# Optimization experiments

Measured on AMD Instinct MI355X. Metric: run time of the kernel, lower is better.

## Reference

```python
import jax, jax.numpy as jnp
import numpy as np
import math

NEG_INF = -10000.0

def setup_inputs() -> dict:
    key = jax.random.key(0)
    k1, k2, k3 = jax.random.split(key, 3)
    B, Sq, Sk, H, D = 2, 2048, 2048, 16, 64
    q = jax.random.normal(k1, (B, Sq, H, D), dtype=jnp.float32)
    kv = jax.random.normal(k2, (B, Sk, 2, H, D), dtype=jnp.float32)
    key_padding_mask = jax.random.randint(k3, (B, Sk), 0, 2).astype(jnp.bool_)
    return {"q": q, "kv": kv, "key_padding_mask": key_padding_mask}

def reference(q, kv, key_padding_mask):
    # q: (B, Sq, H, D); kv: (B, Sk, 2, H, D); key_padding_mask: (B, Sk) True=keep
    D = q.shape[-1]
    softmax_scale = 1.0 / math.sqrt(D)
    k = kv[:, :, 0]  # (B, Sk, H, D)
    v = kv[:, :, 1]  # (B, Sk, H, D)
    # (B, H, Sq, Sk) score matrix
    scores = jnp.einsum('bthd,bshd->bhts', q, k * softmax_scale)
    # additive padding mask: 0 where keep, NEG_INF where masked out
    pad = jnp.where(key_padding_mask, 0.0, NEG_INF).astype(scores.dtype)
    scores = scores + pad[:, None, None, :]
    attention = jax.nn.softmax(scores, axis=-1)
    # dropout_p = 0.0 (eval mode) -> no-op
    output = jnp.einsum('bhts,bshd->bthd', attention, v)
    return output
```

## Files before the change

kernel.cpp:

```cpp
#include <hip/hip_runtime.h>

typedef unsigned short u16;
typedef unsigned int   u32;
typedef u16   u16x8 __attribute__((ext_vector_type(8)));
typedef float f32x4 __attribute__((ext_vector_type(4)));
typedef __bf16 bf16x8 __attribute__((ext_vector_type(8)));
typedef u32   u32x2 __attribute__((ext_vector_type(2)));
typedef u32   u32x4 __attribute__((ext_vector_type(4)));

#define QSCALE  0.18033688011112f
#define BM_OPEN  -28.8539008177793f
#define BM_MASK  -14455.8043097f

__device__ __forceinline__ u16 f2bf(float x){
  __bf16 h = (__bf16)x;
  return __builtin_bit_cast(u16, h);
}
__device__ __forceinline__ f32x4 mfma16x16x32(u16x8 a, u16x8 b, f32x4 c){
  return __builtin_amdgcn_mfma_f32_16x16x32_bf16(
      __builtin_bit_cast(bf16x8, a), __builtin_bit_cast(bf16x8, b), c, 0, 0, 0);
}
__device__ __forceinline__ void gld16(const void* g, void* l){
  __builtin_amdgcn_global_load_lds(
      (const __attribute__((address_space(1))) u32*)g,
      (__attribute__((address_space(3))) u32*)l, 16, 0, 0);
}


__global__ __launch_bounds__(256, 4)
void prepass(const float* __restrict__ KV, const int* __restrict__ MASK,
             u16* __restrict__ IMG, float* __restrict__ BIASM)
{
  const int tid = threadIdx.x;
  const int bid = blockIdx.x;
  const int kt = bid & 31;
  const int h  = (bid >> 5) & 15;
  const int b  = bid >> 9;
  const int kb = kt*64;
  const size_t kv_b = (size_t)b*(2048u*2048u);
  u16* tile = IMG + (size_t)bid * 8192;

  {
    const int skey = tid >> 2, scp = tid & 3;
    const float* kp = KV + kv_b + (size_t)(kb + skey)*2048 + h*64 + 16*scp;
    f32x4 f0 = *(const f32x4*)(kp);
    f32x4 f1 = *(const f32x4*)(kp + 4);
    f32x4 f2 = *(const f32x4*)(kp + 8);
    f32x4 f3 = *(const f32x4*)(kp + 12);
    u16x8 c0, c1;
    #pragma unroll
    for (int e = 0; e < 4; ++e){
      c0[e] = f2bf(f0[e]); c0[e+4] = f2bf(f1[e]);
      c1[e] = f2bf(f2[e]); c1[e+4] = f2bf(f3[e]);
    }
    const int idx0 = skey*64 + (((2*scp) ^ (skey & 7)) << 3);
    *(u16x8*)&tile[idx0]     = c0;
    *(u16x8*)&tile[idx0 ^ 8] = c1;
  }
  {
    const int sdb = tid & 7, ssp = tid >> 3;
    const float* vp = KV + kv_b + (size_t)(kb + 2*ssp)*2048 + 1024 + h*64 + 8*sdb;
    f32x4 r0a = *(const f32x4*)(vp);
    f32x4 r0b = *(const f32x4*)(vp + 4);
    f32x4 r1a = *(const f32x4*)(vp + 2048);
    f32x4 r1b = *(const f32x4*)(vp + 2048 + 4);
    u32* vimg = (u32*)(tile + 4096);
    const int wc = ssp >> 2, wi = ssp & 3;
    #pragma unroll
    for (int j = 0; j < 4; ++j){
      const int d0 = 8*sdb + j;
      const int d1 = d0 + 4;
      vimg[d0*32 + ((wc ^ (d0 & 7)) << 2) + wi] = (u32)f2bf(r0a[j]) | ((u32)f2bf(r1a[j]) << 16);
      vimg[d1*32 + ((wc ^ (d1 & 7)) << 2) + wi] = (u32)f2bf(r0b[j]) | ((u32)f2bf(r1b[j]) << 16);
    }
  }
  if (h == 0 && tid < 64){
    const int s = kb + tid;
    BIASM[b*2048 + s] = MASK[b*2048 + s] ? BM_OPEN : BM_MASK;
  }
}

template<int PRE>
__global__ __launch_bounds__(256, 2)
void attn_main(const float* __restrict__ Q, const float* __restrict__ KV,
               const int* __restrict__ MASK, const u16* __restrict__ IMG,
               const float* __restrict__ BIASM, float* __restrict__ OUT)
{
  __shared__ __align__(16) u16 KVbuf[2][8192];
  __shared__ __align__(16) u32 Pw[4][32*36];

  const int tid  = threadIdx.x;
  const int w    = tid >> 6;
  const int lane = tid & 63;
  const int lg   = lane >> 4;
  const int ln   = lane & 15;

  const int bid0 = blockIdx.x;
  const int bid  = (bid0 & 7)*64 + (bid0 >> 3);
  const int qt  = bid & 15;
  const int h   = (bid >> 4) & 15;
  const int b   = bid >> 8;

  const int qbase = qt*128 + w*32;
  const size_t q_b  = (size_t)b * (2048u*1024u);
  const size_t kv_b = (size_t)b * (2048u*2048u);

  const int lnoff = ln*64;
  const int ck0   = ((lg ^ (ln & 7)) << 3);
  const int ck1   = ck0 ^ 32;

  u16x8 Qf[2][2];
  #pragma unroll
  for (int G = 0; G < 2; ++G){
    const int qrow = qbase + 16*G + ln;
    const float* qp = Q + q_b + (size_t)qrow*1024 + h*64 + 8*lg;
    #pragma unroll
    for (int kc = 0; kc < 2; ++kc){
      f32x4 a = *(const f32x4*)(qp + 32*kc);
      f32x4 c = *(const f32x4*)(qp + 32*kc + 4);
      u16x8 v;
      #pragma unroll
      for (int e = 0; e < 4; ++e){
        v[e]     = f2bf(a[e] * QSCALE);
        v[e + 4] = f2bf(c[e] * QSCALE);
      }
      Qf[G][kc] = v;
    }
  }

  f32x4 Oacc[2][4];
  #pragma unroll
  for (int G = 0; G < 2; ++G)
    #pragma unroll
    for (int dt = 0; dt < 4; ++dt)
      Oacc[G][dt] = f32x4{0.f,0.f,0.f,0.f};
  float lrun[2] = { 0.f, 0.f };

  const char* img0 = (const char*)IMG + (size_t)((b*16 + h)*32) * 16384;
  const int so = tid*16;
  const int skey = tid >> 2, scp = tid & 3;
  const int sdb  = tid & 7,  ssp = tid >> 3;
  const float* kp0 = KV + kv_b + (size_t)skey*2048 + h*64 + 16*scp;
  const float* vp0 = KV + kv_b + (size_t)(2*ssp)*2048 + 1024 + h*64 + 8*sdb;
  f32x4 kf0, kf1, kf2, kf3, va, vb2, vc, vd;

#define STAGE_ISSUE(T, DST) do{                                               \
    if constexpr (PRE){                                                       \
      const char* g_ = img0 + (size_t)(T)*16384;                              \
      char* l_ = (char*)(DST);                                                \
      gld16(g_+so,        l_+so);                                             \
      gld16(g_+so+4096,   l_+so+4096);                                        \
      gld16(g_+so+8192,   l_+so+8192);                                        \
      gld16(g_+so+12288,  l_+so+12288);                                       \
    } else {                                                                  \
      const float* kp_ = kp0 + (size_t)(T)*64*2048;                           \
      kf0=*(const f32x4*)(kp_);   kf1=*(const f32x4*)(kp_+4);                 \
      kf2=*(const f32x4*)(kp_+8); kf3=*(const f32x4*)(kp_+12);                \
      const float* vp_ = vp0 + (size_t)(T)*64*2048;                           \
      va=*(const f32x4*)(vp_);      vb2=*(const f32x4*)(vp_+4);               \
      vc=*(const f32x4*)(vp_+2048); vd =*(const f32x4*)(vp_+2048+4);          \
    }                                                                         \
  }while(0)

#define STAGE_WRITE(DST) do{                                                  \
    u16x8 c0_, c1_;                                                           \
    _Pragma("unroll") for (int e_=0; e_<4; ++e_){                             \
      c0_[e_]=f2bf(kf0[e_]); c0_[e_+4]=f2bf(kf1[e_]);                         \
      c1_[e_]=f2bf(kf2[e_]); c1_[e_+4]=f2bf(kf3[e_]); }                       \
    const int kix_ = skey*64 + (((2*scp) ^ (skey & 7)) << 3);                 \
    *(u16x8*)&(DST)[kix_]     = c0_;                                          \
    *(u16x8*)&(DST)[kix_ ^ 8] = c1_;                                          \
    u32* vimg_ = (u32*)((DST)+4096);                                          \
    const int wc_ = ssp >> 2, wi_ = ssp & 3;                                  \
    _Pragma("unroll") for (int j_=0; j_<4; ++j_){                             \
      const int d0_=8*sdb+j_, d1_=d0_+4;                                      \
      vimg_[d0_*32 + ((wc_ ^ (d0_&7)) << 2) + wi_] = (u32)f2bf(va[j_])  | ((u32)f2bf(vc[j_])<<16); \
      vimg_[d1_*32 + ((wc_ ^ (d1_&7)) << 2) + wi_] = (u32)f2bf(vb2[j_]) | ((u32)f2bf(vd[j_])<<16); \
    }                                                                         \
  }while(0)

  STAGE_ISSUE(0, &KVbuf[0][0]);
  if constexpr (!PRE) { STAGE_WRITE(&KVbuf[0][0]); }
  __syncthreads();

  for (int t = 0; t < 32; ++t){
    const u16* Kb = &KVbuf[t & 1][0];
    const u16* Vb = Kb + 4096;

    if (t < 31) STAGE_ISSUE(t+1, &KVbuf[(t+1) & 1][0]);

    f32x4 S[2][4];
    #pragma unroll
    for (int ct = 0; ct < 4; ++ct){
      f32x4 bv;
      if constexpr (PRE){
        bv = *(const f32x4*)(BIASM + b*2048 + t*64 + 16*ct + 4*lg);
      } else {
        const int4 mv = *(const int4*)(MASK + b*2048 + t*64 + 16*ct + 4*lg);
        bv[0] = mv.x ? BM_OPEN : BM_MASK;
        bv[1] = mv.y ? BM_OPEN : BM_MASK;
        bv[2] = mv.z ? BM_OPEN : BM_MASK;
        bv[3] = mv.w ? BM_OPEN : BM_MASK;
      }
      S[0][ct] = bv;
      S[1][ct] = bv;
    }

    __builtin_amdgcn_s_setprio(1);
    #pragma unroll
    for (int ct = 0; ct < 4; ++ct){
      const int rb = ct*1024 + lnoff;
      u16x8 k0 = *(const u16x8*)&Kb[rb + ck0];
      u16x8 k1 = *(const u16x8*)&Kb[rb + ck1];
      S[0][ct] = mfma16x16x32(k0, Qf[0][0], S[0][ct]);
      S[1][ct] = mfma16x16x32(k0, Qf[1][0], S[1][ct]);
      S[0][ct] = mfma16x16x32(k1, Qf[0][1], S[0][ct]);
      S[1][ct] = mfma16x16x32(k1, Qf[1][1], S[1][ct]);
    }
    __builtin_amdgcn_s_setprio(0);

    #pragma unroll
    for (int G = 0; G < 2; ++G){
      float ps = 0.f;
      #pragma unroll
      for (int ct = 0; ct < 4; ++ct){
        #pragma unroll
        for (int r = 0; r < 4; ++r){
          const float p = __builtin_amdgcn_exp2f(S[G][ct][r]);
          S[G][ct][r] = p;
          ps += p;
        }
      }
      lrun[G] += ps;
      #pragma unroll
      for (int ct = 0; ct < 4; ++ct){
        u32x2 pw;
        pw[0] = (u32)f2bf(S[G][ct][0]) | ((u32)f2bf(S[G][ct][1]) << 16);
        pw[1] = (u32)f2bf(S[G][ct][2]) | ((u32)f2bf(S[G][ct][3]) << 16);
        *(u32x2*)&Pw[w][(16*G + ln)*36 + 8*ct + 2*lg] = pw;
      }
    }

    asm volatile("" ::: "memory");

    u16x8 Pf[2][2];
    #pragma unroll
    for (int G = 0; G < 2; ++G)
      #pragma unroll
      for (int sc = 0; sc < 2; ++sc){
        u32x4 pr = *(const u32x4*)&Pw[w][(16*G + ln)*36 + 4*lg + 16*sc];
        Pf[G][sc] = __builtin_bit_cast(u16x8, pr);
      }

    __builtin_amdgcn_s_setprio(1);
    #pragma unroll
    for (int dt = 0; dt < 4; ++dt){
      const int rb = dt*1024 + lnoff;
      u16x8 v0 = *(const u16x8*)&Vb[rb + ck0];
      u16x8 v1 = *(const u16x8*)&Vb[rb + ck1];
      Oacc[0][dt] = mfma16x16x32(v0, Pf[0][0], Oacc[0][dt]);
      Oacc[1][dt] = mfma16x16x32(v0, Pf[1][0], Oacc[1][dt]);
      Oacc[0][dt] = mfma16x16x32(v1, Pf[0][1], Oacc[0][dt]);
      Oacc[1][dt] = mfma16x16x32(v1, Pf[1][1], Oacc[1][dt]);
    }
    __builtin_amdgcn_s_setprio(0);

    if (t < 31){
      if constexpr (!PRE) { STAGE_WRITE(&KVbuf[(t+1) & 1][0]); }
      __syncthreads();
    }
  }

  #pragma unroll
  for (int G = 0; G < 2; ++G){
    float l_ = lrun[G];
    l_ += __shfl_xor(l_, 16, 64);
    l_ += __shfl_xor(l_, 32, 64);
    const float inv = 1.f / l_;
    const int qrow = qbase + 16*G + ln;
    float* op = OUT + q_b + (size_t)qrow*1024 + h*64;
    #pragma unroll
    for (int dt = 0; dt < 4; ++dt){
      f32x4 ov;
      ov[0] = Oacc[G][dt][0] * inv;
      ov[1] = Oacc[G][dt][1] * inv;
      ov[2] = Oacc[G][dt][2] * inv;
      ov[3] = Oacc[G][dt][3] * inv;
      *(f32x4*)(op + 16*dt + 4*lg) = ov;
    }
  }
#undef STAGE_ISSUE
#undef STAGE_WRITE
}

extern "C" void kernel_launch(void* const* d_in, const int* in_sizes, int n_in,
                              void* d_out, int out_size, void* d_ws, size_t ws_size,
                              hipStream_t stream)
{
  const float* Q  = nullptr;
  const float* KV = nullptr;
  const int*   M  = nullptr;
  for (int i = 0; i < n_in; ++i){
    if      (in_sizes[i] == 4194304) Q  = (const float*)d_in[i];
    else if (in_sizes[i] == 8388608) KV = (const float*)d_in[i];
    else if (in_sizes[i] == 4096)    M  = (const int*)d_in[i];
  }
  if (!Q)  Q  = (const float*)d_in[0];
  if (!KV) KV = (const float*)d_in[1];
  if (!M)  M  = (const int*)d_in[2];
  float* O = (float*)d_out;

  const size_t NEED = 16384ull + 1024ull*16384ull;
  if (ws_size >= NEED){
    float* biasm = (float*)d_ws;
    u16*   img   = (u16*)((char*)d_ws + 16384);
    prepass<<<dim3(1024), dim3(256), 0, stream>>>(KV, M, img, biasm);
    attn_main<1><<<dim3(512), dim3(256), 0, stream>>>(Q, KV, M, img, biasm, O);
  } else {
    attn_main<0><<<dim3(512), dim3(256), 0, stream>>>(Q, KV, M, nullptr, nullptr, O);
  }
}
```

Before: 70.29 us.

## Triple-buffer K/V tiles with async LDS loads and partial vmcnt waits

After: 68.15 us. 3.0% less time.

```diff
diff --git a/kernel.cpp b/kernel.cpp
--- a/kernel.cpp
+++ b/kernel.cpp
@@ -86,7 +86,7 @@
                const int* __restrict__ MASK, const u16* __restrict__ IMG,
                const float* __restrict__ BIASM, float* __restrict__ OUT)
 {
-  __shared__ __align__(16) u16 KVbuf[2][8192];
+  __shared__ __align__(16) u16 KVbuf[3][8192];
   __shared__ __align__(16) u32 Pw[4][32*36];
 
   const int tid  = threadIdx.x;
@@ -145,21 +145,21 @@
   f32x4 kf0, kf1, kf2, kf3, va, vb2, vc, vd;
 
 #define STAGE_ISSUE(T, DST) do{                                               \
-    if constexpr (PRE){                                                       \
-      const char* g_ = img0 + (size_t)(T)*16384;                              \
-      char* l_ = (char*)(DST);                                                \
-      gld16(g_+so,        l_+so);                                             \
-      gld16(g_+so+4096,   l_+so+4096);                                        \
-      gld16(g_+so+8192,   l_+so+8192);                                        \
-      gld16(g_+so+12288,  l_+so+12288);                                       \
-    } else {                                                                  \
-      const float* kp_ = kp0 + (size_t)(T)*64*2048;                           \
-      kf0=*(const f32x4*)(kp_);   kf1=*(const f32x4*)(kp_+4);                 \
-      kf2=*(const f32x4*)(kp_+8); kf3=*(const f32x4*)(kp_+12);                \
-      const float* vp_ = vp0 + (size_t)(T)*64*2048;                           \
-      va=*(const f32x4*)(vp_);      vb2=*(const f32x4*)(vp_+4);               \
-      vc=*(const f32x4*)(vp_+2048); vd =*(const f32x4*)(vp_+2048+4);          \
-    }                                                                         \
+    const char* g_ = img0 + (size_t)(T)*16384;                                \
+    char* l_ = (char*)(DST);                                                  \
+    gld16(g_+so,        l_+so);                                               \
+    gld16(g_+so+4096,   l_+so+4096);                                          \
+    gld16(g_+so+8192,   l_+so+8192);                                          \
+    gld16(g_+so+12288,  l_+so+12288);                                         \
+  }while(0)
+
+#define STAGE_REG(T) do{                                                      \
+    const float* kp_ = kp0 + (size_t)(T)*64*2048;                             \
+    kf0=*(const f32x4*)(kp_);   kf1=*(const f32x4*)(kp_+4);                   \
+    kf2=*(const f32x4*)(kp_+8); kf3=*(const f32x4*)(kp_+12);                  \
+    const float* vp_ = vp0 + (size_t)(T)*64*2048;                             \
+    va=*(const f32x4*)(vp_);      vb2=*(const f32x4*)(vp_+4);                 \
+    vc=*(const f32x4*)(vp_+2048); vd =*(const f32x4*)(vp_+2048+4);            \
   }while(0)
 
 #define STAGE_WRITE(DST) do{                                                  \
@@ -179,95 +179,111 @@
     }                                                                         \
   }while(0)
 
-  STAGE_ISSUE(0, &KVbuf[0][0]);
-  if constexpr (!PRE) { STAGE_WRITE(&KVbuf[0][0]); }
-  __syncthreads();
-
-  for (int t = 0; t < 32; ++t){
-    const u16* Kb = &KVbuf[t & 1][0];
-    const u16* Vb = Kb + 4096;
-
-    if (t < 31) STAGE_ISSUE(t+1, &KVbuf[(t+1) & 1][0]);
-
-    f32x4 S[2][4];
-    #pragma unroll
-    for (int ct = 0; ct < 4; ++ct){
-      f32x4 bv;
-      if constexpr (PRE){
-        bv = *(const f32x4*)(BIASM + b*2048 + t*64 + 16*ct + 4*lg);
-      } else {
-        const int4 mv = *(const int4*)(MASK + b*2048 + t*64 + 16*ct + 4*lg);
-        bv[0] = mv.x ? BM_OPEN : BM_MASK;
-        bv[1] = mv.y ? BM_OPEN : BM_MASK;
-        bv[2] = mv.z ? BM_OPEN : BM_MASK;
-        bv[3] = mv.w ? BM_OPEN : BM_MASK;
+#define COMPUTE(T, CUR) do{                                                   \
+    const u16* Kb_ = (CUR);                                                   \
+    const u16* Vb_ = (CUR) + 4096;                                            \
+    f32x4 S[2][4];                                                            \
+    _Pragma("unroll") for (int ct = 0; ct < 4; ++ct){                         \
+      f32x4 bv;                                                               \
+      if constexpr (PRE){                                                     \
+        bv = *(const f32x4*)(BIASM + b*2048 + (T)*64 + 16*ct + 4*lg);         \
+      } else {                                                                \
+        const int4 mv = *(const int4*)(MASK + b*2048 + (T)*64 + 16*ct + 4*lg);\
+        bv[0] = mv.x ? BM_OPEN : BM_MASK;                                     \
+        bv[1] = mv.y ? BM_OPEN : BM_MASK;                                     \
+        bv[2] = mv.z ? BM_OPEN : BM_MASK;                                     \
+        bv[3] = mv.w ? BM_OPEN : BM_MASK;                                     \
+      }                                                                       \
+      S[0][ct] = bv;                                                          \
+      S[1][ct] = bv;                                                          \
+    }                                                                         \
+    __builtin_amdgcn_s_setprio(1);                                            \
+    _Pragma("unroll") for (int ct = 0; ct < 4; ++ct){                         \
+      const int rb = ct*1024 + lnoff;                                         \
+      u16x8 k0 = *(const u16x8*)&Kb_[rb + ck0];                               \
+      u16x8 k1 = *(const u16x8*)&Kb_[rb + ck1];                               \
+      S[0][ct] = mfma16x16x32(k0, Qf[0][0], S[0][ct]);                        \
+      S[1][ct] = mfma16x16x32(k0, Qf[1][0], S[1][ct]);                        \
+      S[0][ct] = mfma16x16x32(k1, Qf[0][1], S[0][ct]);                        \
+      S[1][ct] = mfma16x16x32(k1, Qf[1][1], S[1][ct]);                        \
+    }                                                                         \
+    __builtin_amdgcn_s_setprio(0);                                            \
+    _Pragma("unroll") for (int G = 0; G < 2; ++G){                            \
+      float ps = 0.f;                                                         \
+      _Pragma("unroll") for (int ct = 0; ct < 4; ++ct){                       \
+        _Pragma("unroll") for (int r = 0; r < 4; ++r){                        \
+          const float p = __builtin_amdgcn_exp2f(S[G][ct][r]);                \
+          S[G][ct][r] = p;                                                    \
+          ps += p;                                                            \
+        }                                                                     \
+      }                                                                       \
+      lrun[G] += ps;                                                          \
+      _Pragma("unroll") for (int ct = 0; ct < 4; ++ct){                       \
+        u32x2 pw;                                                             \
+        pw[0] = (u32)f2bf(S[G][ct][0]) | ((u32)f2bf(S[G][ct][1]) << 16);      \
+        pw[1] = (u32)f2bf(S[G][ct][2]) | ((u32)f2bf(S[G][ct][3]) << 16);      \
+        *(u32x2*)&Pw[w][(16*G + ln)*36 + 8*ct + 2*lg] = pw;                   \
+      }                                                                       \
+    }                                                                         \
+    asm volatile("" ::: "memory");                                            \
+    u16x8 Pf[2][2];                                                           \
+    _Pragma("unroll") for (int G = 0; G < 2; ++G)                             \
+      _Pragma("unroll") for (int sc = 0; sc < 2; ++sc){                       \
+        u32x4 pr = *(const u32x4*)&Pw[w][(16*G + ln)*36 + 4*lg + 16*sc];      \
+        Pf[G][sc] = __builtin_bit_cast(u16x8, pr);                            \
+      }                                                                       \
+    __builtin_amdgcn_s_setprio(1);                                            \
+    _Pragma("unroll") for (int dt = 0; dt < 4; ++dt){                         \
+      const int rb = dt*1024 + lnoff;                                         \
+      u16x8 v0 = *(const u16x8*)&Vb_[rb + ck0];                               \
+      u16x8 v1 = *(const u16x8*)&Vb_[rb + ck1];                               \
+      Oacc[0][dt] = mfma16x16x32(v0, Pf[0][0], Oacc[0][dt]);                  \
+      Oacc[1][dt] = mfma16x16x32(v0, Pf[1][0], Oacc[1][dt]);                  \
+      Oacc[0][dt] = mfma16x16x32(v1, Pf[0][1], Oacc[0][dt]);                  \
+      Oacc[1][dt] = mfma16x16x32(v1, Pf[1][1], Oacc[1][dt]);                  \
+    }                                                                         \
+    __builtin_amdgcn_s_setprio(0);                                            \
+  }while(0)
+
+#define SEAM(N) do{                                                           \
+    __builtin_amdgcn_sched_barrier(0);                                        \
+    asm volatile("s_waitcnt vmcnt(%0)" :: "i"(N) : "memory");                 \
+    __builtin_amdgcn_sched_barrier(0);                                        \
+    __builtin_amdgcn_s_barrier();                                             \
+  }while(0)
+
+#define PITER(T, CUR, FREE) do{                                               \
+    if ((T) + 2 <= 31) STAGE_ISSUE((T)+2, FREE);                              \
+    COMPUTE(T, CUR);                                                          \
+    SEAM(4);                                                                  \
+  }while(0)
+
+  if constexpr (PRE){
+    u16* b0 = &KVbuf[0][0];
+    u16* b1 = &KVbuf[1][0];
+    u16* b2 = &KVbuf[2][0];
+    STAGE_ISSUE(0, b0);
+    STAGE_ISSUE(1, b1);
+    SEAM(4);
+    for (int u = 0; u < 10; ++u){
+      PITER(3*u    , b0, b2);
+      PITER(3*u + 1, b1, b0);
+      PITER(3*u + 2, b2, b1);
+    }
+    COMPUTE(30, b0);
+    SEAM(0);
+    COMPUTE(31, b1);
+  } else {
+    STAGE_REG(0);
+    STAGE_WRITE(&KVbuf[0][0]);
+    __syncthreads();
+    for (int t = 0; t < 32; ++t){
+      if (t < 31) STAGE_REG(t+1);
+      COMPUTE(t, &KVbuf[t & 1][0]);
+      if (t < 31){
+        STAGE_WRITE(&KVbuf[(t+1) & 1][0]);
+        __syncthreads();
       }
-      S[0][ct] = bv;
-      S[1][ct] = bv;
-    }
-
-    __builtin_amdgcn_s_setprio(1);
-    #pragma unroll
-    for (int ct = 0; ct < 4; ++ct){
-      const int rb = ct*1024 + lnoff;
-      u16x8 k0 = *(const u16x8*)&Kb[rb + ck0];
-      u16x8 k1 = *(const u16x8*)&Kb[rb + ck1];
-      S[0][ct] = mfma16x16x32(k0, Qf[0][0], S[0][ct]);
-      S[1][ct] = mfma16x16x32(k0, Qf[1][0], S[1][ct]);
-      S[0][ct] = mfma16x16x32(k1, Qf[0][1], S[0][ct]);
-      S[1][ct] = mfma16x16x32(k1, Qf[1][1], S[1][ct]);
-    }
-    __builtin_amdgcn_s_setprio(0);
-
-    #pragma unroll
-    for (int G = 0; G < 2; ++G){
-      float ps = 0.f;
-      #pragma unroll
-      for (int ct = 0; ct < 4; ++ct){
-        #pragma unroll
-        for (int r = 0; r < 4; ++r){
-          const float p = __builtin_amdgcn_exp2f(S[G][ct][r]);
-          S[G][ct][r] = p;
-          ps += p;
-        }
-      }
-      lrun[G] += ps;
-      #pragma unroll
-      for (int ct = 0; ct < 4; ++ct){
-        u32x2 pw;
-        pw[0] = (u32)f2bf(S[G][ct][0]) | ((u32)f2bf(S[G][ct][1]) << 16);
-        pw[1] = (u32)f2bf(S[G][ct][2]) | ((u32)f2bf(S[G][ct][3]) << 16);
-        *(u32x2*)&Pw[w][(16*G + ln)*36 + 8*ct + 2*lg] = pw;
-      }
-    }
-
-    asm volatile("" ::: "memory");
-
-    u16x8 Pf[2][2];
-    #pragma unroll
-    for (int G = 0; G < 2; ++G)
-      #pragma unroll
-      for (int sc = 0; sc < 2; ++sc){
-        u32x4 pr = *(const u32x4*)&Pw[w][(16*G + ln)*36 + 4*lg + 16*sc];
-        Pf[G][sc] = __builtin_bit_cast(u16x8, pr);
-      }
-
-    __builtin_amdgcn_s_setprio(1);
-    #pragma unroll
-    for (int dt = 0; dt < 4; ++dt){
-      const int rb = dt*1024 + lnoff;
-      u16x8 v0 = *(const u16x8*)&Vb[rb + ck0];
-      u16x8 v1 = *(const u16x8*)&Vb[rb + ck1];
-      Oacc[0][dt] = mfma16x16x32(v0, Pf[0][0], Oacc[0][dt]);
-      Oacc[1][dt] = mfma16x16x32(v0, Pf[1][0], Oacc[1][dt]);
-      Oacc[0][dt] = mfma16x16x32(v1, Pf[0][1], Oacc[0][dt]);
-      Oacc[1][dt] = mfma16x16x32(v1, Pf[1][1], Oacc[1][dt]);
-    }
-    __builtin_amdgcn_s_setprio(0);
-
-    if (t < 31){
-      if constexpr (!PRE) { STAGE_WRITE(&KVbuf[(t+1) & 1][0]); }
-      __syncthreads();
     }
   }
 
@@ -290,7 +306,11 @@
     }
   }
 #undef STAGE_ISSUE
+#undef STAGE_REG
 #undef STAGE_WRITE
+#undef COMPUTE
+#undef SEAM
+#undef PITER
 }
 
 extern "C" void kernel_launch(void* const* d_in, const int* in_sizes, int n_in,
```
